# Performance work log

Measured on AMD Instinct MI355X. Metric: run time of the kernel, lower is better.

The kernel has to match this reference:

```python
import jax, jax.numpy as jnp
import numpy as np

D_MODEL = 1024
N_HEADS = 16
HEAD_DIM = D_MODEL // N_HEADS
D_FF = 4096
LN_EPS = 1e-5


def _layernorm(x, g, b):
    mu = jnp.mean(x, axis=-1, keepdims=True)
    var = jnp.var(x, axis=-1, keepdims=True)
    return (x - mu) * jax.lax.rsqrt(var + LN_EPS) * g + b


def setup_inputs() -> dict:
    key = jax.random.key(0)
    ks = jax.random.split(key, 10)
    s = 0.02
    return {
        "hidden_states": jax.random.normal(ks[0], (2, 2048, D_MODEL), dtype=jnp.float32),
        "qkv_w": jax.random.normal(ks[1], (3 * D_MODEL, D_MODEL), dtype=jnp.float32) * s,
        "qkv_b": jnp.zeros((3 * D_MODEL,), dtype=jnp.float32),
        "out_w": jax.random.normal(ks[2], (D_MODEL, D_MODEL), dtype=jnp.float32) * s,
        "out_b": jnp.zeros((D_MODEL,), dtype=jnp.float32),
        "fc1_w": jax.random.normal(ks[3], (D_FF, D_MODEL), dtype=jnp.float32) * s,
        "fc1_b": jnp.zeros((D_FF,), dtype=jnp.float32),
        "fc2_w": jax.random.normal(ks[4], (D_MODEL, D_FF), dtype=jnp.float32) * s,
        "fc2_b": jnp.zeros((D_MODEL,), dtype=jnp.float32),
        "ln1_g": jnp.ones((D_MODEL,), dtype=jnp.float32),
        "ln1_b": jnp.zeros((D_MODEL,), dtype=jnp.float32),
        "ln2_g": jnp.ones((D_MODEL,), dtype=jnp.float32),
        "ln2_b": jnp.zeros((D_MODEL,), dtype=jnp.float32),
    }


def reference(hidden_states, qkv_w, qkv_b, out_w, out_b, fc1_w, fc1_b, fc2_w, fc2_b, ln1_g, ln1_b, ln2_g, ln2_b):
    B, S, D = hidden_states.shape
    scale = 1.0 / np.sqrt(HEAD_DIM).astype(np.float32)

    normed = _layernorm(hidden_states, ln1_g, ln1_b)
    qkv = normed @ qkv_w.T + qkv_b  # [B,S,3D]
    qkv = qkv.reshape(B, S, 3, N_HEADS, HEAD_DIM).transpose(2, 0, 3, 1, 4)
    q, k, v = qkv[0], qkv[1], qkv[2]  # [B,H,S,hd]

    scores = jnp.einsum("bhqd,bhkd->bhqk", q, k) * scale
    causal = jnp.tril(jnp.ones((S, S), dtype=bool))
    scores = jnp.where(causal, scores, jnp.float32(-jnp.inf))
    probs = jax.nn.softmax(scores, axis=-1)
    attn = jnp.einsum("bhqk,bhkd->bhqd", probs, v)  # [B,H,S,hd]
    attn = attn.transpose(0, 2, 1, 3).reshape(B, S, D)
    attn = attn @ out_w.T + out_b

    hidden = hidden_states + attn
    normed2 = _layernorm(hidden, ln2_g, ln2_b)
    ff = jax.nn.gelu(normed2 @ fc1_w.T + fc1_b, approximate=False)
    ff = ff @ fc2_w.T + fc2_b
    return hidden + ff
```

## Files before the change

### kernel.cpp

```cpp
#include <hip/hip_runtime.h>
#include <math.h>

using bf16   = __bf16;
using bf16x8 = __attribute__((ext_vector_type(8))) __bf16;
using bf16x4 = __attribute__((ext_vector_type(4))) __bf16;
using f32x4  = __attribute__((ext_vector_type(4))) float;
using f32x16 = __attribute__((ext_vector_type(16))) float;
using uint2v = __attribute__((ext_vector_type(2))) unsigned int;

#define MFMA_16x16x32(a, b, c) __builtin_amdgcn_mfma_f32_16x16x32_bf16((a), (b), (c), 0, 0, 0)
#define MFMA32(a, b, c) __builtin_amdgcn_mfma_f32_32x32x16_bf16((a), (b), (c), 0, 0, 0)

__device__ __forceinline__ void gll16(const void* g, void* l) {
  __builtin_amdgcn_global_load_lds((const __attribute__((address_space(1))) void*)g,
                                   (__attribute__((address_space(3))) void*)l,
                                   16, 0, 0);
}

__device__ __forceinline__ int cvtpk(float lo, float hi) {
  int r;
  asm("v_cvt_pk_bf16_f32 %0, %1, %2" : "=v"(r) : "v"(lo), "v"(hi));
  return r;
}

__device__ __forceinline__ float gelu_fast(float x) {
  const float u = 0.7978845608f * __builtin_fmaf(0.044715f * x, x * x, x);
  const float e = exp2f(2.885390082f * u);
  return x * e / (e + 1.f);
}

__global__ __launch_bounds__(256) void cast4_kernel(const float* __restrict__ s0, bf16* d0,
                                                    const float* __restrict__ s1, bf16* d1,
                                                    const float* __restrict__ s2, bf16* d2,
                                                    const float* __restrict__ s3, bf16* d3) {
  int i = blockIdx.x * 256 + threadIdx.x;
  const float* s;
  bf16* d;
  if (i < 786432) { s = s0; d = d0; }
  else if (i < 1048576) { s = s1; d = d1; i -= 786432; }
  else if (i < 2097152) { s = s2; d = d2; i -= 1048576; }
  else { s = s3; d = d3; i -= 2097152; }
  float4 v = ((const float4*)s)[i];
  bf16x4 o;
  o[0] = (bf16)v.x; o[1] = (bf16)v.y; o[2] = (bf16)v.z; o[3] = (bf16)v.w;
  ((bf16x4*)d)[i] = o;
}

template <typename T>
__global__ __launch_bounds__(256) void ln_kernel(const T* __restrict__ x,
                                                 const float* __restrict__ g,
                                                 const float* __restrict__ b,
                                                 bf16* __restrict__ out) {
  const int row = blockIdx.x, t = threadIdx.x;
  float4 v;
  if constexpr (sizeof(T) == 4) {
    v = ((const float4*)((const float*)x + (size_t)row * 1024))[t];
  } else {
    const bf16x4 raw = ((const bf16x4*)((const bf16*)x + (size_t)row * 1024))[t];
    v.x = (float)raw[0]; v.y = (float)raw[1]; v.z = (float)raw[2]; v.w = (float)raw[3];
  }
  float s1 = v.x + v.y + v.z + v.w;
  float s2 = v.x * v.x + v.y * v.y + v.z * v.z + v.w * v.w;
#pragma unroll
  for (int d = 32; d; d >>= 1) {
    s1 += __shfl_xor(s1, d);
    s2 += __shfl_xor(s2, d);
  }
  __shared__ float red[8];
  const int w = t >> 6;
  if ((t & 63) == 0) { red[w] = s1; red[4 + w] = s2; }
  __syncthreads();
  s1 = red[0] + red[1] + red[2] + red[3];
  s2 = red[4] + red[5] + red[6] + red[7];
  const float mu = s1 * (1.f / 1024.f);
  const float rstd = rsqrtf(s2 * (1.f / 1024.f) - mu * mu + 1e-5f);
  const float4 gv = ((const float4*)g)[t];
  const float4 bv = ((const float4*)b)[t];
  bf16x4 o;
  o[0] = (bf16)((v.x - mu) * rstd * gv.x + bv.x);
  o[1] = (bf16)((v.y - mu) * rstd * gv.y + bv.y);
  o[2] = (bf16)((v.z - mu) * rstd * gv.z + bv.z);
  o[3] = (bf16)((v.w - mu) * rstd * gv.w + bv.w);
  ((bf16x4*)(out + (size_t)row * 1024))[t] = o;
}

template <int EPI>
__global__ __launch_bounds__(512, 2) void gemm256(const bf16* __restrict__ A,
                                                  const bf16* __restrict__ W,
                                                  const float* __restrict__ bias,
                                                  bf16* __restrict__ outp,
                                                  bf16* __restrict__ vout, int N, int K,
                                                  int nbx) {
  __shared__ __align__(1024) bf16 lds[65536];
  const int t = threadIdx.x, lane = t & 63, w = t >> 6;
  const int wm = w >> 2, wn = w & 3;
  const int l15 = lane & 15, lg = lane >> 4;

  const int nwg = gridDim.x, cpx = nwg >> 3, bid = blockIdx.x;
  const int swz = (bid & 7) * cpx + (bid >> 3);
  const int bx = swz % nbx, by = swz / nbx;
  const int m0 = by * 256, n0 = bx * 256;

  const bf16* src[8];
  int dst[8];
  {
    const int ss[2] = {t, t + 512};
#pragma unroll
    for (int i = 0; i < 2; i++) {
      const int d = ss[i] * 16;
      const int L = d ^ (((d >> 9) & 1) << 5);
      const int r = L >> 7, coff = (L & 127) >> 1;
#pragma unroll
      for (int hf = 0; hf < 2; hf++) {
        src[hf * 2 + i]     = A + (size_t)(m0 + hf * 128 + r) * K + coff;
        src[4 + hf * 2 + i] = W + (size_t)(n0 + hf * 128 + r) * K + coff;
        dst[hf * 2 + i]     = hf * 8192 + ss[i] * 8;
        dst[4 + hf * 2 + i] = 16384 + hf * 8192 + ss[i] * 8;
      }
    }
  }

#define STAGE256(db_)                                   \
  do {                                                  \
    _Pragma("unroll") for (int u = 0; u < 8; u++) {     \
      gll16(src[u], lds + (db_)*32768 + dst[u]);        \
      src[u] += 64;                                     \
    }                                                   \
  } while (0)

  f32x4 acc[8][4];
#pragma unroll
  for (int mi = 0; mi < 8; mi++)
#pragma unroll
    for (int ni = 0; ni < 4; ni++) acc[mi][ni] = (f32x4){0.f, 0.f, 0.f, 0.f};

  const int ntiles = K >> 6;
  STAGE256(0);
  asm volatile("s_waitcnt vmcnt(0)" ::: "memory");
  __builtin_amdgcn_s_barrier();

  for (int kt = 0; kt < ntiles; ++kt) {
    const int db = kt & 1;
    const bf16* Ab = lds + db * 32768 + wm * 8192;
    const bf16* Bb = lds + db * 32768 + 16384 + (wn >> 1) * 8192;
    bf16x8 bfr[4][2];
#pragma unroll
    for (int p = 0; p < 4; ++p) {
      bf16x8 af[2][2];
#pragma unroll
      for (int mi2 = 0; mi2 < 2; ++mi2)
#pragma unroll
        for (int ks = 0; ks < 2; ++ks) {
          const int row = (2 * p + mi2) * 16 + l15;
          const int Pb = (row * 128 + ks * 64 + lg * 16) ^ (((row >> 2) & 1) << 5);
          af[mi2][ks] = *(const bf16x8*)((const char*)Ab + Pb);
        }
      if (p == 0) {
#pragma unroll
        for (int ni = 0; ni < 4; ++ni)
#pragma unroll
          for (int ks = 0; ks < 2; ++ks) {
            const int row = (wn & 1) * 64 + ni * 16 + l15;
            const int Pb = (row * 128 + ks * 64 + lg * 16) ^ (((row >> 2) & 1) << 5);
            bfr[ni][ks] = *(const bf16x8*)((const char*)Bb + Pb);
          }
        if (kt + 1 < ntiles) STAGE256(db ^ 1);
      }
      __builtin_amdgcn_s_barrier();
      asm volatile("s_waitcnt lgkmcnt(0)" ::: "memory");
      __builtin_amdgcn_sched_barrier(0);
      __builtin_amdgcn_s_setprio(1);
#pragma unroll
      for (int ks = 0; ks < 2; ++ks)
#pragma unroll
        for (int ni = 0; ni < 4; ++ni) {
          acc[2 * p][ni] = MFMA_16x16x32(af[0][ks], bfr[ni][ks], acc[2 * p][ni]);
          acc[2 * p + 1][ni] = MFMA_16x16x32(af[1][ks], bfr[ni][ks], acc[2 * p + 1][ni]);
        }
      __builtin_amdgcn_s_setprio(0);
      if (p == 3) asm volatile("s_waitcnt vmcnt(0)" ::: "memory");
      __builtin_amdgcn_s_barrier();
    }
  }
#undef STAGE256

#pragma unroll
  for (int mi = 0; mi < 8; ++mi) {
    const int row0 = m0 + wm * 128 + mi * 16 + lg * 4;
#pragma unroll
    for (int ni = 0; ni < 4; ++ni) {
      const int col = n0 + wn * 64 + ni * 16 + l15;
      const float bc = bias[col];
      if (EPI == 0 && col >= 2048) {
        bf16x4 ov;
#pragma unroll
        for (int r = 0; r < 4; ++r) ov[r] = (bf16)(acc[mi][ni][r] + bc);
        const int bb = row0 >> 11, s = row0 & 2047, dc = col - 2048;
        *(bf16x4*)(vout + ((size_t)(bb * 16 + (dc >> 6)) * 64 + (dc & 63)) * 2048 + s) = ov;
      } else {
#pragma unroll
        for (int r = 0; r < 4; ++r) {
          float v = acc[mi][ni][r] + bc;
          if (EPI == 1) v = gelu_fast(v);
          outp[(size_t)(row0 + r) * N + col] = (bf16)v;
        }
      }
    }
  }
}

template <int MODE>
__global__ __launch_bounds__(512, 4) void gemm128(const bf16* __restrict__ A,
                                                  const bf16* __restrict__ W,
                                                  const float* __restrict__ bias,
                                                  const void* __restrict__ residv,
                                                  void* __restrict__ outv, int N, int K,
                                                  int nbx) {
  __shared__ __align__(1024) bf16 lds[32768];
  const int t = threadIdx.x, lane = t & 63, w = t >> 6;
  const int wm = w >> 2, wn = w & 3;
  const int l15 = lane & 15, lg = lane >> 4;

  const int nwg = gridDim.x, cpx = nwg >> 3, bid = blockIdx.x;
  const int swz = (bid & 7) * cpx + (bid >> 3);
  const int bx = swz % nbx, by = swz / nbx;
  const int m0 = by * 128, n0 = bx * 128;

  const bf16* src[4];
  int dst[4];
#pragma unroll
  for (int u = 0; u < 2; ++u) {
    const int off = u * 8192 + t * 16;
    const int row = off >> 7, slot = (off >> 4) & 7;
    const int col = (slot ^ (row & 7)) * 8;
    src[u]     = A + (size_t)(m0 + row) * K + col;
    src[2 + u] = W + (size_t)(n0 + row) * K + col;
    dst[u]     = off >> 1;
    dst[2 + u] = 8192 + (off >> 1);
  }

#define STAGE128(db_)                                   \
  do {                                                  \
    _Pragma("unroll") for (int u = 0; u < 4; u++) {     \
      gll16(src[u], lds + (db_)*16384 + dst[u]);        \
      src[u] += 64;                                     \
    }                                                   \
  } while (0)

  f32x4 acc[4][2];
#pragma unroll
  for (int mi = 0; mi < 4; mi++)
#pragma unroll
    for (int ni = 0; ni < 2; ni++) acc[mi][ni] = (f32x4){0.f, 0.f, 0.f, 0.f};

  const int ntiles = K >> 6;
  STAGE128(0);
  asm volatile("s_waitcnt vmcnt(0)" ::: "memory");
  __builtin_amdgcn_s_barrier();

  for (int kt = 0; kt < ntiles; ++kt) {
    const int db = kt & 1;
    const char* Ab = (const char*)lds + db * 32768;
    const char* Bb = Ab + 16384;
#pragma unroll
    for (int p = 0; p < 2; ++p) {
      bf16x8 af[4], bfr[2];
#pragma unroll
      for (int mi = 0; mi < 4; ++mi) {
        const int row = wm * 64 + mi * 16 + l15;
        af[mi] = *(const bf16x8*)(Ab + row * 128 + (((p * 4 + lg) ^ (row & 7)) << 4));
      }
#pragma unroll
      for (int ni = 0; ni < 2; ++ni) {
        const int row = wn * 32 + ni * 16 + l15;
        bfr[ni] = *(const bf16x8*)(Bb + row * 128 + (((p * 4 + lg) ^ (row & 7)) << 4));
      }
      if (p == 0 && kt + 1 < ntiles) STAGE128(db ^ 1);
      __builtin_amdgcn_s_barrier();
      asm volatile("s_waitcnt lgkmcnt(0)" ::: "memory");
      __builtin_amdgcn_sched_barrier(0);
      __builtin_amdgcn_s_setprio(1);
#pragma unroll
      for (int mi = 0; mi < 4; ++mi)
#pragma unroll
        for (int ni = 0; ni < 2; ++ni)
          acc[mi][ni] = MFMA_16x16x32(af[mi], bfr[ni], acc[mi][ni]);
      __builtin_amdgcn_s_setprio(0);
      if (p == 1) asm volatile("s_waitcnt vmcnt(0)" ::: "memory");
      __builtin_amdgcn_s_barrier();
    }
  }
#undef STAGE128

#pragma unroll
  for (int mi = 0; mi < 4; ++mi) {
    const int row0 = m0 + wm * 64 + mi * 16 + lg * 4;
#pragma unroll
    for (int ni = 0; ni < 2; ++ni) {
      const int col = n0 + wn * 32 + ni * 16 + l15;
      const float bc = bias[col];
#pragma unroll
      for (int r = 0; r < 4; ++r) {
        const size_t idx = (size_t)(row0 + r) * N + col;
        float v = acc[mi][ni][r] + bc;
        if (MODE == 0) {
          v += ((const float*)residv)[idx];
          ((bf16*)outv)[idx] = (bf16)v;
        } else {
          v += (float)((const bf16*)residv)[idx];
          ((float*)outv)[idx] = v;
        }
      }
    }
  }
}

__global__ __launch_bounds__(256) void attn_kernel(const bf16* __restrict__ qkv,
                                                   const bf16* __restrict__ vt,
                                                   bf16* __restrict__ attn_out) {
  __shared__ bf16 Ks[3][4096];
  __shared__ bf16 Vs[3][4096];
  const int t = threadIdx.x, lane = t & 63, w = t >> 6;
  const int l31 = lane & 31, lh = lane >> 5;
  const int bx = blockIdx.x, by = blockIdx.y;
  const int b = by >> 4, h = by & 15;
  const int g = (bx + by) & 15;
  const int qb = (by < 16) ? g : 15 - g;
  const int qw = qb * 128 + w * 32;
  const int qq = qw + l31;
  const int nt = 2 * qb + 2;

  const float cs = 0.18033688011112042f;

  bf16x8 qf[4];
  {
    const bf16* qp = qkv + (size_t)(b * 2048 + qq) * 3072 + h * 64 + lh * 8;
#pragma unroll
    for (int c = 0; c < 4; ++c) qf[c] = *(const bf16x8*)(qp + c * 16);
  }

  const int r0 = t >> 3, c16 = t & 7;
  const int swsl = 8 * (c16 ^ (r0 & 7));
  const bf16* kp0 = qkv + (size_t)(b * 2048 + r0) * 3072 + 1024 + h * 64 + swsl;
  const bf16* kp1 = qkv + (size_t)(b * 2048 + r0 + 32) * 3072 + 1024 + h * 64 + swsl;
  const bf16* vp0 = vt + ((size_t)by * 64 + r0) * 2048 + swsl;
  const bf16* vp1 = vp0 + (size_t)32 * 2048;

#define ASTAGE(buf)                          \
  do {                                       \
    gll16(kp0, &Ks[buf][t * 8]);             \
    gll16(kp1, &Ks[buf][2048 + t * 8]);      \
    gll16(vp0, &Vs[buf][t * 8]);             \
    gll16(vp1, &Vs[buf][2048 + t * 8]);      \
    kp0 += (size_t)64 * 3072;                \
    kp1 += (size_t)64 * 3072;                \
    vp0 += 64;                               \
    vp1 += 64;                               \
  } while (0)

  const f32x16 z16 = {0.f, 0.f, 0.f, 0.f, 0.f, 0.f, 0.f, 0.f,
                      0.f, 0.f, 0.f, 0.f, 0.f, 0.f, 0.f, 0.f};
  f32x16 o0a = z16, o0b = z16, o1a = z16, o1b = z16;
  float lsum = 0.f;

  ASTAGE(0);
  ASTAGE(1);
  int b0 = 0, b1 = 1, b2 = 2;
  for (int tt = 0; tt < nt; ++tt) {
    const int kv0 = tt * 64;
    if (tt < nt - 1) asm volatile("s_waitcnt vmcnt(4)" ::: "memory");
    else             asm volatile("s_waitcnt vmcnt(0)" ::: "memory");
    __builtin_amdgcn_s_barrier();
    if (tt + 2 < nt) ASTAGE(b2);
    if (kv0 <= qw + 31) {
      const bf16* kbp = Ks[b0];
      const bf16* vbp = Vs[b0];
      const bool up = (kv0 + 32) <= (qw + 31);
      f32x16 s0v = z16, s1v = z16;
      __builtin_amdgcn_s_setprio(1);
#pragma unroll
      for (int c = 0; c < 4; ++c) {
        const int slot = ((c * 2 + lh) ^ (l31 & 7)) * 16;
        const bf16x8 a0 = *(const bf16x8*)((const char*)kbp + l31 * 128 + slot);
        s0v = MFMA32(a0, qf[c], s0v);
      }
      if (up) {
#pragma unroll
        for (int c = 0; c < 4; ++c) {
          const int slot = ((c * 2 + lh) ^ (l31 & 7)) * 16;
          const bf16x8 a1 = *(const bf16x8*)((const char*)kbp + (32 + l31) * 128 + slot);
          s1v = MFMA32(a1, qf[c], s1v);
        }
      }
      __builtin_amdgcn_s_setprio(0);
      if (kv0 + 64 > qw) {
#pragma unroll
        for (int j = 0; j < 16; ++j) {
          const int kr = kv0 + (j & 3) + 8 * (j >> 2) + 4 * lh;
          if (kr > qq) s0v[j] = -1e30f;
          if (kr + 32 > qq) s1v[j] = -1e30f;
        }
      }
#pragma unroll
      for (int j = 0; j < 16; ++j) {
        s0v[j] = exp2f(s0v[j] * cs);
        lsum += s0v[j];
      }
      if (up) {
#pragma unroll
        for (int j = 0; j < 16; ++j) {
          s1v[j] = exp2f(s1v[j] * cs);
          lsum += s1v[j];
        }
      }
      unsigned int w0[8];
#pragma unroll
      for (int j = 0; j < 8; ++j) w0[j] = (unsigned int)cvtpk(s0v[2 * j], s0v[2 * j + 1]);
#define PVHALF2(WW, KB, OA, OB)                                                      \
  do {                                                                               \
    const uint2v e0 = __builtin_amdgcn_permlane32_swap(WW[0], WW[2], false, false);  \
    const uint2v e1 = __builtin_amdgcn_permlane32_swap(WW[1], WW[3], false, false);  \
    const uint2v e2 = __builtin_amdgcn_permlane32_swap(WW[4], WW[6], false, false);  \
    const uint2v e3 = __builtin_amdgcn_permlane32_swap(WW[5], WW[7], false, false);  \
    union { unsigned int i[4]; bf16x8 v; } pA, pB;                                   \
    pA.i[0] = e0[0]; pA.i[1] = e1[0]; pA.i[2] = e0[1]; pA.i[3] = e1[1];              \
    pB.i[0] = e2[0]; pB.i[1] = e3[0]; pB.i[2] = e2[1]; pB.i[3] = e3[1];              \
    const int sA = (((KB)*4 + lh) ^ (l31 & 7)) * 16;                                 \
    const int sB = (((KB)*4 + 2 + lh) ^ (l31 & 7)) * 16;                             \
    const bf16x8 vA0 = *(const bf16x8*)((const char*)vbp + l31 * 128 + sA);          \
    const bf16x8 vA1 = *(const bf16x8*)((const char*)vbp + (32 + l31) * 128 + sA);   \
    const bf16x8 vB0 = *(const bf16x8*)((const char*)vbp + l31 * 128 + sB);          \
    const bf16x8 vB1 = *(const bf16x8*)((const char*)vbp + (32 + l31) * 128 + sB);   \
    OA = MFMA32(vA0, pA.v, OA);                                                      \
    OB = MFMA32(vA1, pA.v, OB);                                                      \
    OA = MFMA32(vB0, pB.v, OA);                                                      \
    OB = MFMA32(vB1, pB.v, OB);                                                      \
  } while (0)
      __builtin_amdgcn_s_setprio(1);
      PVHALF2(w0, 0, o0a, o1a);
      __builtin_amdgcn_s_setprio(0);
      if (up) {
        unsigned int w1[8];
#pragma unroll
        for (int j = 0; j < 8; ++j) w1[j] = (unsigned int)cvtpk(s1v[2 * j], s1v[2 * j + 1]);
        __builtin_amdgcn_s_setprio(1);
        PVHALF2(w1, 1, o0b, o1b);
        __builtin_amdgcn_s_setprio(0);
      }
#undef PVHALF2
    }
    const int tmp = b0; b0 = b1; b1 = b2; b2 = tmp;
  }
#undef ASTAGE

  lsum += __shfl_xor(lsum, 32);
  const float rinv = 1.f / lsum;
  const f32x16 oacc0 = o0a + o0b, oacc1 = o1a + o1b;
  bf16* op = attn_out + (size_t)(b * 2048 + qq) * 1024 + h * 64;
#pragma unroll
  for (int gR = 0; gR < 4; ++gR) {
    bf16x4 o0, o1;
#pragma unroll
    for (int r = 0; r < 4; ++r) {
      o0[r] = (bf16)(oacc0[4 * gR + r] * rinv);
      o1[r] = (bf16)(oacc1[4 * gR + r] * rinv);
    }
    *(bf16x4*)(op + 8 * gR + 4 * lh) = o0;
    *(bf16x4*)(op + 32 + 8 * gR + 4 * lh) = o1;
  }
}

extern "C" void kernel_launch(void* const* d_in, const int* in_sizes, int n_in,
                              void* d_out, int out_size, void* d_ws, size_t ws_size,
                              hipStream_t stream) {
  (void)in_sizes; (void)n_in; (void)out_size; (void)ws_size;
  const float* hidden = (const float*)d_in[0];
  const float* qkv_w  = (const float*)d_in[1];
  const float* qkv_b  = (const float*)d_in[2];
  const float* out_w  = (const float*)d_in[3];
  const float* out_b  = (const float*)d_in[4];
  const float* fc1_w  = (const float*)d_in[5];
  const float* fc1_b  = (const float*)d_in[6];
  const float* fc2_w  = (const float*)d_in[7];
  const float* fc2_b  = (const float*)d_in[8];
  const float* ln1_g  = (const float*)d_in[9];
  const float* ln1_b  = (const float*)d_in[10];
  const float* ln2_g  = (const float*)d_in[11];
  const float* ln2_b  = (const float*)d_in[12];
  float* outp = (float*)d_out;

  char* ws = (char*)d_ws;
  bf16*  ln1o  = (bf16*)(ws);
  bf16*  qkvb  = (bf16*)(ws + ((size_t)8 << 20));
  bf16*  vtb   = (bf16*)(ws + ((size_t)32 << 20));
  bf16*  atto  = (bf16*)(ws + ((size_t)40 << 20));
  bf16*  res1b = (bf16*)(ws + ((size_t)48 << 20));
  bf16*  ln2o  = (bf16*)(ws + ((size_t)64 << 20));
  bf16*  ff1   = (bf16*)(ws + ((size_t)72 << 20));
  bf16*  wqkv  = (bf16*)(ws + ((size_t)104 << 20));
  bf16*  wout  = (bf16*)(ws + ((size_t)110 << 20));
  bf16*  wfc1  = (bf16*)(ws + ((size_t)112 << 20));
  bf16*  wfc2  = (bf16*)(ws + ((size_t)120 << 20));

  cast4_kernel<<<12288, 256, 0, stream>>>(qkv_w, wqkv, out_w, wout, fc1_w, wfc1, fc2_w, wfc2);

  ln_kernel<float><<<4096, 256, 0, stream>>>(hidden, ln1_g, ln1_b, ln1o);
  gemm256<0><<<192, 512, 0, stream>>>(ln1o, wqkv, qkv_b, qkvb, vtb, 3072, 1024, 12);
  attn_kernel<<<dim3(16, 32), 256, 0, stream>>>(qkvb, vtb, atto);
  gemm128<0><<<256, 512, 0, stream>>>(atto, wout, out_b, hidden, res1b, 1024, 1024, 8);
  ln_kernel<bf16><<<4096, 256, 0, stream>>>(res1b, ln2_g, ln2_b, ln2o);
  gemm256<1><<<256, 512, 0, stream>>>(ln2o, wfc1, fc1_b, ff1, nullptr, 4096, 1024, 16);
  gemm128<1><<<256, 512, 0, stream>>>(ff1, wfc2, fc2_b, res1b, outp, 1024, 4096, 8);
}
```

Before: 234.7 us.

## Process 64 queries per wave in attention, halving grid and doubling K/V reuse

Each wave in the attention kernel now computes two 32-query row groups (A and B) against every 64-key K/V tile loaded into LDS. Each block therefore covers 256 queries, and the grid shrinks from 16x32 to 8x32 blocks. The aim is to double the reuse of each staged K/V tile and each LDS fragment read, and to cut the share of tiles that need causal masking. In exchange there are fewer blocks, the earlier pairing that balanced causal work across blocks is gone, and launch_bounds(256,1) raises per-thread register use to hold the doubled score and accumulator state.

```diff
diff --git a/kernel.cpp b/kernel.cpp
--- a/kernel.cpp
+++ b/kernel.cpp
@@ -315,28 +315,31 @@
   }
 }
 
-__global__ __launch_bounds__(256) void attn_kernel(const bf16* __restrict__ qkv,
-                                                   const bf16* __restrict__ vt,
-                                                   bf16* __restrict__ attn_out) {
+__global__ __launch_bounds__(256, 1) void attn_kernel(const bf16* __restrict__ qkv,
+                                                      const bf16* __restrict__ vt,
+                                                      bf16* __restrict__ attn_out) {
   __shared__ bf16 Ks[3][4096];
   __shared__ bf16 Vs[3][4096];
   const int t = threadIdx.x, lane = t & 63, w = t >> 6;
   const int l31 = lane & 31, lh = lane >> 5;
   const int bx = blockIdx.x, by = blockIdx.y;
   const int b = by >> 4, h = by & 15;
-  const int g = (bx + by) & 15;
-  const int qb = (by < 16) ? g : 15 - g;
-  const int qw = qb * 128 + w * 32;
-  const int qq = qw + l31;
-  const int nt = 2 * qb + 2;
+  const int qb = (bx + by) & 7;
+  const int qw = qb * 256 + w * 64;
+  const int qqA = qw + l31, qqB = qqA + 32;
+  const int nt = 4 * qb + 4;
 
   const float cs = 0.18033688011112042f;
 
-  bf16x8 qf[4];
+  bf16x8 qfA[4], qfB[4];
   {
-    const bf16* qp = qkv + (size_t)(b * 2048 + qq) * 3072 + h * 64 + lh * 8;
-#pragma unroll
-    for (int c = 0; c < 4; ++c) qf[c] = *(const bf16x8*)(qp + c * 16);
+    const bf16* qpA = qkv + (size_t)(b * 2048 + qqA) * 3072 + h * 64 + lh * 8;
+    const bf16* qpB = qkv + (size_t)(b * 2048 + qqB) * 3072 + h * 64 + lh * 8;
+#pragma unroll
+    for (int c = 0; c < 4; ++c) {
+      qfA[c] = *(const bf16x8*)(qpA + c * 16);
+      qfB[c] = *(const bf16x8*)(qpB + c * 16);
+    }
   }
 
   const int r0 = t >> 3, c16 = t & 7;
@@ -360,8 +363,8 @@
 
   const f32x16 z16 = {0.f, 0.f, 0.f, 0.f, 0.f, 0.f, 0.f, 0.f,
                       0.f, 0.f, 0.f, 0.f, 0.f, 0.f, 0.f, 0.f};
-  f32x16 o0a = z16, o0b = z16, o1a = z16, o1b = z16;
-  float lsum = 0.f;
+  f32x16 oA0 = z16, oA1 = z16, oB0 = z16, oB1 = z16;
+  float lsA = 0.f, lsB = 0.f;
 
   ASTAGE(0);
   ASTAGE(1);
@@ -372,101 +375,108 @@
     else             asm volatile("s_waitcnt vmcnt(0)" ::: "memory");
     __builtin_amdgcn_s_barrier();
     if (tt + 2 < nt) ASTAGE(b2);
-    if (kv0 <= qw + 31) {
+    if (kv0 <= qw) {
       const bf16* kbp = Ks[b0];
       const bf16* vbp = Vs[b0];
-      const bool up = (kv0 + 32) <= (qw + 31);
-      f32x16 s0v = z16, s1v = z16;
+      const bool last = (kv0 == qw);
+      f32x16 sA0 = z16, sA1 = z16, sB0 = z16, sB1 = z16;
       __builtin_amdgcn_s_setprio(1);
 #pragma unroll
       for (int c = 0; c < 4; ++c) {
         const int slot = ((c * 2 + lh) ^ (l31 & 7)) * 16;
         const bf16x8 a0 = *(const bf16x8*)((const char*)kbp + l31 * 128 + slot);
-        s0v = MFMA32(a0, qf[c], s0v);
-      }
-      if (up) {
-#pragma unroll
-        for (int c = 0; c < 4; ++c) {
-          const int slot = ((c * 2 + lh) ^ (l31 & 7)) * 16;
-          const bf16x8 a1 = *(const bf16x8*)((const char*)kbp + (32 + l31) * 128 + slot);
-          s1v = MFMA32(a1, qf[c], s1v);
-        }
+        const bf16x8 a1 = *(const bf16x8*)((const char*)kbp + (32 + l31) * 128 + slot);
+        sA0 = MFMA32(a0, qfA[c], sA0);
+        sB0 = MFMA32(a0, qfB[c], sB0);
+        sB1 = MFMA32(a1, qfB[c], sB1);
+        sA1 = MFMA32(a1, qfA[c], sA1);
       }
       __builtin_amdgcn_s_setprio(0);
-      if (kv0 + 64 > qw) {
+      if (last) {
 #pragma unroll
         for (int j = 0; j < 16; ++j) {
           const int kr = kv0 + (j & 3) + 8 * (j >> 2) + 4 * lh;
-          if (kr > qq) s0v[j] = -1e30f;
-          if (kr + 32 > qq) s1v[j] = -1e30f;
+          if (kr > qqA) sA0[j] = -1e30f;
+          sA1[j] = -1e30f;
+          if (kr + 32 > qqB) sB1[j] = -1e30f;
         }
       }
 #pragma unroll
       for (int j = 0; j < 16; ++j) {
-        s0v[j] = exp2f(s0v[j] * cs);
-        lsum += s0v[j];
-      }
-      if (up) {
-#pragma unroll
-        for (int j = 0; j < 16; ++j) {
-          s1v[j] = exp2f(s1v[j] * cs);
-          lsum += s1v[j];
-        }
-      }
-      unsigned int w0[8];
-#pragma unroll
-      for (int j = 0; j < 8; ++j) w0[j] = (unsigned int)cvtpk(s0v[2 * j], s0v[2 * j + 1]);
-#define PVHALF2(WW, KB, OA, OB)                                                      \
+        sA0[j] = exp2f(sA0[j] * cs);
+        sA1[j] = exp2f(sA1[j] * cs);
+        sB0[j] = exp2f(sB0[j] * cs);
+        sB1[j] = exp2f(sB1[j] * cs);
+        lsA += sA0[j] + sA1[j];
+        lsB += sB0[j] + sB1[j];
+      }
+      unsigned int wvA0[8], wvA1[8], wvB0[8], wvB1[8];
+#pragma unroll
+      for (int j = 0; j < 8; ++j) {
+        wvA0[j] = (unsigned int)cvtpk(sA0[2 * j], sA0[2 * j + 1]);
+        wvA1[j] = (unsigned int)cvtpk(sA1[2 * j], sA1[2 * j + 1]);
+        wvB0[j] = (unsigned int)cvtpk(sB0[2 * j], sB0[2 * j + 1]);
+        wvB1[j] = (unsigned int)cvtpk(sB1[2 * j], sB1[2 * j + 1]);
+      }
+#define PVDUAL(WA, WB, KB)                                                           \
   do {                                                                               \
-    const uint2v e0 = __builtin_amdgcn_permlane32_swap(WW[0], WW[2], false, false);  \
-    const uint2v e1 = __builtin_amdgcn_permlane32_swap(WW[1], WW[3], false, false);  \
-    const uint2v e2 = __builtin_amdgcn_permlane32_swap(WW[4], WW[6], false, false);  \
-    const uint2v e3 = __builtin_amdgcn_permlane32_swap(WW[5], WW[7], false, false);  \
-    union { unsigned int i[4]; bf16x8 v; } pA, pB;                                   \
-    pA.i[0] = e0[0]; pA.i[1] = e1[0]; pA.i[2] = e0[1]; pA.i[3] = e1[1];              \
-    pB.i[0] = e2[0]; pB.i[1] = e3[0]; pB.i[2] = e2[1]; pB.i[3] = e3[1];              \
+    const uint2v eA0 = __builtin_amdgcn_permlane32_swap(WA[0], WA[2], false, false); \
+    const uint2v eA1 = __builtin_amdgcn_permlane32_swap(WA[1], WA[3], false, false); \
+    const uint2v eA2 = __builtin_amdgcn_permlane32_swap(WA[4], WA[6], false, false); \
+    const uint2v eA3 = __builtin_amdgcn_permlane32_swap(WA[5], WA[7], false, false); \
+    const uint2v eB0 = __builtin_amdgcn_permlane32_swap(WB[0], WB[2], false, false); \
+    const uint2v eB1 = __builtin_amdgcn_permlane32_swap(WB[1], WB[3], false, false); \
+    const uint2v eB2 = __builtin_amdgcn_permlane32_swap(WB[4], WB[6], false, false); \
+    const uint2v eB3 = __builtin_amdgcn_permlane32_swap(WB[5], WB[7], false, false); \
+    union { unsigned int i[4]; bf16x8 v; } pA1, pB1, pA2, pB2;                       \
+    pA1.i[0] = eA0[0]; pA1.i[1] = eA1[0]; pA1.i[2] = eA0[1]; pA1.i[3] = eA1[1];      \
+    pB1.i[0] = eA2[0]; pB1.i[1] = eA3[0]; pB1.i[2] = eA2[1]; pB1.i[3] = eA3[1];      \
+    pA2.i[0] = eB0[0]; pA2.i[1] = eB1[0]; pA2.i[2] = eB0[1]; pA2.i[3] = eB1[1];      \
+    pB2.i[0] = eB2[0]; pB2.i[1] = eB3[0]; pB2.i[2] = eB2[1]; pB2.i[3] = eB3[1];      \
     const int sA = (((KB)*4 + lh) ^ (l31 & 7)) * 16;                                 \
     const int sB = (((KB)*4 + 2 + lh) ^ (l31 & 7)) * 16;                             \
     const bf16x8 vA0 = *(const bf16x8*)((const char*)vbp + l31 * 128 + sA);          \
     const bf16x8 vA1 = *(const bf16x8*)((const char*)vbp + (32 + l31) * 128 + sA);   \
     const bf16x8 vB0 = *(const bf16x8*)((const char*)vbp + l31 * 128 + sB);          \
     const bf16x8 vB1 = *(const bf16x8*)((const char*)vbp + (32 + l31) * 128 + sB);   \
-    OA = MFMA32(vA0, pA.v, OA);                                                      \
-    OB = MFMA32(vA1, pA.v, OB);                                                      \
-    OA = MFMA32(vB0, pB.v, OA);                                                      \
-    OB = MFMA32(vB1, pB.v, OB);                                                      \
+    oA0 = MFMA32(vA0, pA1.v, oA0);                                                   \
+    oA1 = MFMA32(vA1, pA1.v, oA1);                                                   \
+    oB0 = MFMA32(vA0, pA2.v, oB0);                                                   \
+    oB1 = MFMA32(vA1, pA2.v, oB1);                                                   \
+    oA0 = MFMA32(vB0, pB1.v, oA0);                                                   \
+    oA1 = MFMA32(vB1, pB1.v, oA1);                                                   \
+    oB0 = MFMA32(vB0, pB2.v, oB0);                                                   \
+    oB1 = MFMA32(vB1, pB2.v, oB1);                                                   \
   } while (0)
       __builtin_amdgcn_s_setprio(1);
-      PVHALF2(w0, 0, o0a, o1a);
+      PVDUAL(wvA0, wvB0, 0);
+      PVDUAL(wvA1, wvB1, 1);
       __builtin_amdgcn_s_setprio(0);
-      if (up) {
-        unsigned int w1[8];
-#pragma unroll
-        for (int j = 0; j < 8; ++j) w1[j] = (unsigned int)cvtpk(s1v[2 * j], s1v[2 * j + 1]);
-        __builtin_amdgcn_s_setprio(1);
-        PVHALF2(w1, 1, o0b, o1b);
-        __builtin_amdgcn_s_setprio(0);
-      }
-#undef PVHALF2
+#undef PVDUAL
     }
     const int tmp = b0; b0 = b1; b1 = b2; b2 = tmp;
   }
 #undef ASTAGE
 
-  lsum += __shfl_xor(lsum, 32);
-  const float rinv = 1.f / lsum;
-  const f32x16 oacc0 = o0a + o0b, oacc1 = o1a + o1b;
-  bf16* op = attn_out + (size_t)(b * 2048 + qq) * 1024 + h * 64;
+  lsA += __shfl_xor(lsA, 32);
+  lsB += __shfl_xor(lsB, 32);
+  const float riA = 1.f / lsA, riB = 1.f / lsB;
+  bf16* opA = attn_out + (size_t)(b * 2048 + qqA) * 1024 + h * 64;
+  bf16* opB = attn_out + (size_t)(b * 2048 + qqB) * 1024 + h * 64;
 #pragma unroll
   for (int gR = 0; gR < 4; ++gR) {
-    bf16x4 o0, o1;
+    bf16x4 a0, a1, c0, c1;
 #pragma unroll
     for (int r = 0; r < 4; ++r) {
-      o0[r] = (bf16)(oacc0[4 * gR + r] * rinv);
-      o1[r] = (bf16)(oacc1[4 * gR + r] * rinv);
-    }
-    *(bf16x4*)(op + 8 * gR + 4 * lh) = o0;
-    *(bf16x4*)(op + 32 + 8 * gR + 4 * lh) = o1;
+      a0[r] = (bf16)(oA0[4 * gR + r] * riA);
+      a1[r] = (bf16)(oA1[4 * gR + r] * riA);
+      c0[r] = (bf16)(oB0[4 * gR + r] * riB);
+      c1[r] = (bf16)(oB1[4 * gR + r] * riB);
+    }
+    *(bf16x4*)(opA + 8 * gR + 4 * lh) = a0;
+    *(bf16x4*)(opA + 32 + 8 * gR + 4 * lh) = a1;
+    *(bf16x4*)(opB + 8 * gR + 4 * lh) = c0;
+    *(bf16x4*)(opB + 32 + 8 * gR + 4 * lh) = c1;
   }
 }
 
@@ -506,7 +516,7 @@
 
   ln_kernel<float><<<4096, 256, 0, stream>>>(hidden, ln1_g, ln1_b, ln1o);
   gemm256<0><<<192, 512, 0, stream>>>(ln1o, wqkv, qkv_b, qkvb, vtb, 3072, 1024, 12);
-  attn_kernel<<<dim3(16, 32), 256, 0, stream>>>(qkvb, vtb, atto);
+  attn_kernel<<<dim3(8, 32), 256, 0, stream>>>(qkvb, vtb, atto);
   gemm128<0><<<256, 512, 0, stream>>>(atto, wout, out_b, hidden, res1b, 1024, 1024, 8);
   ln_kernel<bf16><<<4096, 256, 0, stream>>>(res1b, ln2_g, ln2_b, ln2o);
   gemm256<1><<<256, 512, 0, stream>>>(ln2o, wfc1, fc1_b, ff1, nullptr, 4096, 1024, 16);
```

Measured after the change: 254.4 us. 8.4% more time.
